# Kernel tuning notes

Measured on AMD Instinct MI355X. Metric: run time of the kernel, lower is better.

Reference implementation:

```python
import jax, jax.numpy as jnp
import numpy as np

MARGIN = 0.5
CURV = 1.0
B, D = 8192, 128
N_CLASSES = 256


def setup_inputs() -> dict:
    key = jax.random.key(0)
    k1, k2, k3 = jax.random.split(key, 3)
    emb = jax.random.normal(k1, (B, D), dtype=jnp.float32)
    # project onto Poincare ball: random radii in (0, 0.8) so all norms < 1
    radii = 0.8 * jax.random.uniform(k2, (B, 1), dtype=jnp.float32)
    emb = emb / (jnp.linalg.norm(emb, axis=-1, keepdims=True) + 1e-6) * radii
    labels = jax.random.randint(k3, (B,), 0, N_CLASSES, dtype=jnp.int64)
    return {"embeddings": emb, "labels": labels}


def _poincare_dist_matrix(x, c):
    # d(x,y) = arccosh(1 + 2c||x-y||^2 / ((1-c||x||^2)(1-c||y||^2))) / sqrt(c)
    sq = jnp.sum(x * x, axis=-1)                       # (B,)
    gram = x @ x.T                                      # (B,B) GEMM
    d2 = jnp.maximum(sq[:, None] + sq[None, :] - 2.0 * gram, 0.0)
    denom = (1.0 - c * sq)[:, None] * (1.0 - c * sq)[None, :]
    arg = 1.0 + 2.0 * c * d2 / denom
    # clamp slightly above 1: arccosh grad is infinite at 1 (diagonal / identical pts)
    return jnp.arccosh(jnp.maximum(arg, 1.0 + 1e-7)) / jnp.sqrt(c)


def reference(embeddings, labels):
    dist = _poincare_dist_matrix(embeddings, CURV)      # (B,B)
    same = labels[:, None] == labels[None, :]
    eye = jnp.eye(labels.shape[0], dtype=bool)
    pos_mask = same & ~eye
    neg_mask = ~same
    has_pos = jnp.any(pos_mask, axis=1)
    has_neg = jnp.any(neg_mask, axis=1)
    valid = has_pos & has_neg
    d_pos = jnp.max(jnp.where(pos_mask, dist, -jnp.inf), axis=1)
    d_neg = jnp.min(jnp.where(neg_mask, dist, jnp.inf), axis=1)
    d_pos = jnp.where(has_pos, d_pos, 0.0)
    d_neg = jnp.where(has_neg, d_neg, 0.0)
    l = jnp.maximum(d_pos - d_neg + MARGIN, 0.0)
    l = jnp.where(valid, l, 0.0)
    cnt = jnp.sum(valid)
    return jnp.where(cnt > 0, jnp.sum(l) / jnp.maximum(cnt, 1), 0.0)
```

## Files before the change

kernel.cpp:

```cpp
#include <hip/hip_runtime.h>
#include <hip/hip_bf16.h>

typedef __attribute__((ext_vector_type(8))) __bf16 bf16x8;
typedef __attribute__((ext_vector_type(4))) float f32x4;
typedef unsigned short u16;

#define NB 8192
#define ND 128
#define NCHUNK 8

__device__ inline u16 f2b(float f){
  __hip_bfloat16 h = __float2bfloat16(f);
  return *reinterpret_cast<u16*>(&h);
}

extern "C" __global__ __launch_bounds__(256)
void prep_k(const float* __restrict__ x, u16* __restrict__ xb,
            float* __restrict__ sq, float* __restrict__ pinv)
{
  const int tid = blockIdx.x * 256 + threadIdx.x;
  const int row = tid >> 5;
  const int sub = tid & 31;
  const float4 v = reinterpret_cast<const float4*>(x)[row * 32 + sub];
  float s = v.x*v.x + v.y*v.y + v.z*v.z + v.w*v.w;
  #pragma unroll
  for (int m = 1; m < 32; m <<= 1) s += __shfl_xor(s, m, 32);
  ushort4 o;
  o.x = f2b(v.x); o.y = f2b(v.y); o.z = f2b(v.z); o.w = f2b(v.w);
  reinterpret_cast<ushort4*>(xb)[row * 32 + sub] = o;
  if (sub == 0){ sq[row] = s; pinv[row] = 1.0f / (1.0f - s); }
}

extern "C" __global__ __launch_bounds__(256, 2)
void gram_k(const u16* __restrict__ xb, const float* __restrict__ sq,
            const float* __restrict__ pinv, const int* __restrict__ lab,
            float* __restrict__ ppos, float* __restrict__ pneg)
{
  __shared__ u16 Bt[128 * 128];
  const int wid  = threadIdx.x >> 6;
  const int lane = threadIdx.x & 63;
  const int m16  = lane & 15;
  const int quad = lane >> 4;
  const int R0 = blockIdx.x * 128;
  const int C0 = blockIdx.y * 1024;
  const int WR0 = R0 + wid * 32;

  bf16x8 afrag[2][4];
  #pragma unroll
  for (int mt = 0; mt < 2; ++mt){
    const u16* arow = xb + (WR0 + mt*16 + m16) * ND;
    #pragma unroll
    for (int ks = 0; ks < 4; ++ks)
      afrag[mt][ks] = *reinterpret_cast<const bf16x8*>(arow + ks*32 + quad*8);
  }

  float sqi[8]; int labi[8];
  #pragma unroll
  for (int mt = 0; mt < 2; ++mt)
    #pragma unroll
    for (int r = 0; r < 4; ++r){
      const int row = WR0 + mt*16 + quad*4 + r;
      sqi[mt*4+r]  = sq[row];
      labi[mt*4+r] = lab[row];
    }

  float vpos[8], vneg[8];
  #pragma unroll
  for (int i = 0; i < 8; ++i){ vpos[i] = -__builtin_inff(); vneg[i] = __builtin_inff(); }

  for (int ct = 0; ct < 8; ++ct){
    const int CT0 = C0 + ct * 128;
    __syncthreads();
    #pragma unroll
    for (int c = 0; c < 8; ++c){
      const int cc   = wid * 8 + c;
      const int brow = cc * 4 + (lane >> 4);
      const int src  = (lane & 15) ^ (brow & 15);
      const u16* gsrc = xb + (CT0 + brow) * ND + src * 8;
      __builtin_amdgcn_global_load_lds(
          (__attribute__((address_space(1))) void*)gsrc,
          (__attribute__((address_space(3))) void*)(Bt + cc * 512), 16, 0, 0);
    }
    __syncthreads();

    f32x4 acc[2][8];
    #pragma unroll
    for (int mt = 0; mt < 2; ++mt)
      #pragma unroll
      for (int nt = 0; nt < 8; ++nt){
        f32x4 z = {0.f, 0.f, 0.f, 0.f};
        acc[mt][nt] = z;
      }

    #pragma unroll
    for (int ks = 0; ks < 4; ++ks){
      const int t = ks * 4 + quad;
      #pragma unroll
      for (int nt = 0; nt < 8; ++nt){
        const bf16x8 bfrag = *reinterpret_cast<const bf16x8*>(
            Bt + (nt*16 + m16) * 128 + ((t ^ m16) * 8));
        acc[0][nt] = __builtin_amdgcn_mfma_f32_16x16x32_bf16(afrag[0][ks], bfrag, acc[0][nt], 0, 0, 0);
        acc[1][nt] = __builtin_amdgcn_mfma_f32_16x16x32_bf16(afrag[1][ks], bfrag, acc[1][nt], 0, 0, 0);
      }
    }

    #pragma unroll
    for (int nt = 0; nt < 8; ++nt){
      const int col  = CT0 + nt*16 + m16;
      const float sqj = sq[col];
      const float pj  = pinv[col];
      const int  labj = lab[col];
      #pragma unroll
      for (int mt = 0; mt < 2; ++mt){
        const bool tilediag = (WR0 + mt*16) == (CT0 + nt*16);
        #pragma unroll
        for (int r = 0; r < 4; ++r){
          const float g = acc[mt][nt][r];
          float u = fmaf(-2.0f, g, sqi[mt*4+r] + sqj);
          u = fmaxf(u, 0.0f) * pj;
          const bool same = (labi[mt*4+r] == labj);
          const bool dg   = tilediag && (m16 == quad*4 + r);
          const int idx = mt*4 + r;
          if (same && !dg) vpos[idx] = fmaxf(vpos[idx], u);
          if (!same)       vneg[idx] = fminf(vneg[idx], u);
        }
      }
    }
  }

  #pragma unroll
  for (int i = 0; i < 8; ++i){
    #pragma unroll
    for (int m = 1; m < 16; m <<= 1){
      vpos[i] = fmaxf(vpos[i], __shfl_xor(vpos[i], m, 16));
      vneg[i] = fminf(vneg[i], __shfl_xor(vneg[i], m, 16));
    }
  }
  if (m16 == 0){
    #pragma unroll
    for (int i = 0; i < 8; ++i){
      const int row = WR0 + (i >> 2)*16 + quad*4 + (i & 3);
      ppos[blockIdx.y * NB + row] = vpos[i];
      pneg[blockIdx.y * NB + row] = vneg[i];
    }
  }
}

extern "C" __global__ __launch_bounds__(1024)
void finalize_k(const float* __restrict__ ppos, const float* __restrict__ pneg,
                const float* __restrict__ pinv, float* __restrict__ out)
{
  float lsum = 0.0f; int lcnt = 0;
  for (int row = threadIdx.x; row < NB; row += 1024){
    float up = -__builtin_inff(), un = __builtin_inff();
    #pragma unroll
    for (int c = 0; c < NCHUNK; ++c){
      up = fmaxf(up, ppos[c * NB + row]);
      un = fminf(un, pneg[c * NB + row]);
    }
    const bool hp = (up > -__builtin_inff());
    const bool hn = (un <  __builtin_inff());
    const float pi = pinv[row];
    float dp = 0.0f, dn = 0.0f;
    if (hp){ float t = fmaxf(2.0f * up * pi, 1e-7f); dp = log1pf(t + sqrtf(t * (t + 2.0f))); }
    if (hn){ float t = fmaxf(2.0f * un * pi, 1e-7f); dn = log1pf(t + sqrtf(t * (t + 2.0f))); }
    if (hp && hn){ lsum += fmaxf(dp - dn + 0.5f, 0.0f); lcnt++; }
  }
  #pragma unroll
  for (int m = 1; m < 64; m <<= 1){
    lsum += __shfl_xor(lsum, m, 64);
    lcnt += __shfl_xor(lcnt, m, 64);
  }
  __shared__ float s_sum[16];
  __shared__ int   s_cnt[16];
  const int w = threadIdx.x >> 6;
  if ((threadIdx.x & 63) == 0){ s_sum[w] = lsum; s_cnt[w] = lcnt; }
  __syncthreads();
  if (threadIdx.x == 0){
    float S = 0.0f; int C = 0;
    for (int i = 0; i < 16; ++i){ S += s_sum[i]; C += s_cnt[i]; }
    out[0] = (C > 0) ? (S / (float)C) : 0.0f;
  }
}

extern "C" void kernel_launch(void* const* d_in, const int* in_sizes, int n_in,
                              void* d_out, int out_size, void* d_ws, size_t ws_size,
                              hipStream_t stream)
{
  const float* x  = (const float*)d_in[0];
  const int* lab  = (const int*)d_in[1];
  char* ws = (char*)d_ws;
  u16*  xb   = (u16*)ws;
  float* sq   = (float*)(ws + 2*1024*1024);
  float* pinv = (float*)(ws + 2*1024*1024 + 32*1024);
  float* ppos = (float*)(ws + 2*1024*1024 + 64*1024);
  float* pneg = (float*)(ws + 2*1024*1024 + 64*1024 + 256*1024);

  hipLaunchKernelGGL(prep_k, dim3(1024), dim3(256), 0, stream, x, xb, sq, pinv);
  hipLaunchKernelGGL(gram_k, dim3(64, NCHUNK), dim3(256), 0, stream,
                     xb, sq, pinv, lab, ppos, pneg);
  hipLaunchKernelGGL(finalize_k, dim3(1), dim3(1024), 0, stream, ppos, pneg, pinv, (float*)d_out);
}
```

Baseline: 116.7 us.

## Double gram grid chunks, pack column params, split epilogue, parallelize finalize

```diff
diff --git a/kernel.cpp b/kernel.cpp
--- a/kernel.cpp
+++ b/kernel.cpp
@@ -7,7 +7,9 @@
 
 #define NB 8192
 #define ND 128
-#define NCHUNK 8
+#define NCHUNK 16
+#define NEGINF (-__builtin_inff())
+#define POSINF (__builtin_inff())
 
 __device__ inline u16 f2b(float f){
   __hip_bfloat16 h = __float2bfloat16(f);
@@ -15,8 +17,8 @@
 }
 
 extern "C" __global__ __launch_bounds__(256)
-void prep_k(const float* __restrict__ x, u16* __restrict__ xb,
-            float* __restrict__ sq, float* __restrict__ pinv)
+void prep_k(const float* __restrict__ x, const int* __restrict__ lab,
+            u16* __restrict__ xb, float4* __restrict__ colp)
 {
   const int tid = blockIdx.x * 256 + threadIdx.x;
   const int row = tid >> 5;
@@ -28,12 +30,14 @@
   ushort4 o;
   o.x = f2b(v.x); o.y = f2b(v.y); o.z = f2b(v.z); o.w = f2b(v.w);
   reinterpret_cast<ushort4*>(xb)[row * 32 + sub] = o;
-  if (sub == 0){ sq[row] = s; pinv[row] = 1.0f / (1.0f - s); }
-}
-
-extern "C" __global__ __launch_bounds__(256, 2)
-void gram_k(const u16* __restrict__ xb, const float* __restrict__ sq,
-            const float* __restrict__ pinv, const int* __restrict__ lab,
+  if (sub == 0){
+    const float p = 1.0f / (1.0f - s);
+    colp[row] = make_float4(s, p, s * p, __int_as_float(lab[row]));
+  }
+}
+
+extern "C" __global__ __launch_bounds__(256, 4)
+void gram_k(const u16* __restrict__ xb, const float4* __restrict__ colp,
             float* __restrict__ ppos, float* __restrict__ pneg)
 {
   __shared__ u16 Bt[128 * 128];
@@ -41,8 +45,8 @@
   const int lane = threadIdx.x & 63;
   const int m16  = lane & 15;
   const int quad = lane >> 4;
-  const int R0 = blockIdx.x * 128;
-  const int C0 = blockIdx.y * 1024;
+  const int R0  = blockIdx.x * 128;
+  const int C0  = blockIdx.y * 512;
   const int WR0 = R0 + wid * 32;
 
   bf16x8 afrag[2][4];
@@ -59,23 +63,23 @@
   for (int mt = 0; mt < 2; ++mt)
     #pragma unroll
     for (int r = 0; r < 4; ++r){
-      const int row = WR0 + mt*16 + quad*4 + r;
-      sqi[mt*4+r]  = sq[row];
-      labi[mt*4+r] = lab[row];
+      const float4 cp = colp[WR0 + mt*16 + quad*4 + r];
+      sqi[mt*4+r]  = cp.x;
+      labi[mt*4+r] = __float_as_int(cp.w);
     }
 
   float vpos[8], vneg[8];
   #pragma unroll
-  for (int i = 0; i < 8; ++i){ vpos[i] = -__builtin_inff(); vneg[i] = __builtin_inff(); }
-
-  for (int ct = 0; ct < 8; ++ct){
+  for (int i = 0; i < 8; ++i){ vpos[i] = NEGINF; vneg[i] = POSINF; }
+
+  for (int ct = 0; ct < 4; ++ct){
     const int CT0 = C0 + ct * 128;
     __syncthreads();
     #pragma unroll
     for (int c = 0; c < 8; ++c){
       const int cc   = wid * 8 + c;
-      const int brow = cc * 4 + (lane >> 4);
-      const int src  = (lane & 15) ^ (brow & 15);
+      const int brow = cc * 4 + quad;
+      const int src  = m16 ^ (brow & 15);
       const u16* gsrc = xb + (CT0 + brow) * ND + src * 8;
       __builtin_amdgcn_global_load_lds(
           (__attribute__((address_space(1))) void*)gsrc,
@@ -83,46 +87,61 @@
     }
     __syncthreads();
 
-    f32x4 acc[2][8];
-    #pragma unroll
-    for (int mt = 0; mt < 2; ++mt)
+    #pragma unroll
+    for (int half = 0; half < 2; ++half){
+      f32x4 acc[2][4];
       #pragma unroll
-      for (int nt = 0; nt < 8; ++nt){
-        f32x4 z = {0.f, 0.f, 0.f, 0.f};
-        acc[mt][nt] = z;
+      for (int mt = 0; mt < 2; ++mt)
+        #pragma unroll
+        for (int nt4 = 0; nt4 < 4; ++nt4){
+          f32x4 z = {0.f, 0.f, 0.f, 0.f};
+          acc[mt][nt4] = z;
+        }
+
+      #pragma unroll
+      for (int ks = 0; ks < 4; ++ks){
+        const int t = ks * 4 + quad;
+        #pragma unroll
+        for (int nt4 = 0; nt4 < 4; ++nt4){
+          const int nt = half * 4 + nt4;
+          const bf16x8 bfrag = *reinterpret_cast<const bf16x8*>(
+              Bt + (nt*16 + m16) * 128 + ((t ^ m16) * 8));
+          acc[0][nt4] = __builtin_amdgcn_mfma_f32_16x16x32_bf16(afrag[0][ks], bfrag, acc[0][nt4], 0, 0, 0);
+          acc[1][nt4] = __builtin_amdgcn_mfma_f32_16x16x32_bf16(afrag[1][ks], bfrag, acc[1][nt4], 0, 0, 0);
+        }
       }
 
-    #pragma unroll
-    for (int ks = 0; ks < 4; ++ks){
-      const int t = ks * 4 + quad;
       #pragma unroll
-      for (int nt = 0; nt < 8; ++nt){
-        const bf16x8 bfrag = *reinterpret_cast<const bf16x8*>(
-            Bt + (nt*16 + m16) * 128 + ((t ^ m16) * 8));
-        acc[0][nt] = __builtin_amdgcn_mfma_f32_16x16x32_bf16(afrag[0][ks], bfrag, acc[0][nt], 0, 0, 0);
-        acc[1][nt] = __builtin_amdgcn_mfma_f32_16x16x32_bf16(afrag[1][ks], bfrag, acc[1][nt], 0, 0, 0);
-      }
-    }
-
-    #pragma unroll
-    for (int nt = 0; nt < 8; ++nt){
-      const int col  = CT0 + nt*16 + m16;
-      const float sqj = sq[col];
-      const float pj  = pinv[col];
-      const int  labj = lab[col];
-      #pragma unroll
-      for (int mt = 0; mt < 2; ++mt){
-        const bool tilediag = (WR0 + mt*16) == (CT0 + nt*16);
+      for (int nt4 = 0; nt4 < 4; ++nt4){
+        const int nt  = half * 4 + nt4;
+        const float4 cp = colp[CT0 + nt*16 + m16];
+        const float pj   = cp.y;
+        const float spj  = cp.z;
+        const int   labj = __float_as_int(cp.w);
+        const float n2pj = -2.0f * pj;
         #pragma unroll
-        for (int r = 0; r < 4; ++r){
-          const float g = acc[mt][nt][r];
-          float u = fmaf(-2.0f, g, sqi[mt*4+r] + sqj);
-          u = fmaxf(u, 0.0f) * pj;
-          const bool same = (labi[mt*4+r] == labj);
-          const bool dg   = tilediag && (m16 == quad*4 + r);
-          const int idx = mt*4 + r;
-          if (same && !dg) vpos[idx] = fmaxf(vpos[idx], u);
-          if (!same)       vneg[idx] = fminf(vneg[idx], u);
+        for (int mt = 0; mt < 2; ++mt){
+          const bool tilediag = (WR0 + mt*16) == (CT0 + nt*16);
+          if (!tilediag){
+            #pragma unroll
+            for (int r = 0; r < 4; ++r){
+              const int idx = mt*4 + r;
+              const float u = fmaf(n2pj, acc[mt][nt4][r], fmaf(sqi[idx], pj, spj));
+              const bool sm = (labi[idx] == labj);
+              vpos[idx] = fmaxf(vpos[idx], sm ? u : NEGINF);
+              vneg[idx] = fminf(vneg[idx], sm ? POSINF : u);
+            }
+          } else {
+            #pragma unroll
+            for (int r = 0; r < 4; ++r){
+              const int idx = mt*4 + r;
+              const float u = fmaf(n2pj, acc[mt][nt4][r], fmaf(sqi[idx], pj, spj));
+              const bool sm = (labi[idx] == labj);
+              const bool dg = (m16 == quad*4 + r);
+              vpos[idx] = fmaxf(vpos[idx], (sm && !dg) ? u : NEGINF);
+              vneg[idx] = fminf(vneg[idx], sm ? POSINF : u);
+            }
+          }
         }
       }
     }
@@ -146,41 +165,49 @@
   }
 }
 
-extern "C" __global__ __launch_bounds__(1024)
-void finalize_k(const float* __restrict__ ppos, const float* __restrict__ pneg,
-                const float* __restrict__ pinv, float* __restrict__ out)
-{
-  float lsum = 0.0f; int lcnt = 0;
-  for (int row = threadIdx.x; row < NB; row += 1024){
-    float up = -__builtin_inff(), un = __builtin_inff();
-    #pragma unroll
-    for (int c = 0; c < NCHUNK; ++c){
-      up = fmaxf(up, ppos[c * NB + row]);
-      un = fminf(un, pneg[c * NB + row]);
-    }
-    const bool hp = (up > -__builtin_inff());
-    const bool hn = (un <  __builtin_inff());
-    const float pi = pinv[row];
-    float dp = 0.0f, dn = 0.0f;
-    if (hp){ float t = fmaxf(2.0f * up * pi, 1e-7f); dp = log1pf(t + sqrtf(t * (t + 2.0f))); }
-    if (hn){ float t = fmaxf(2.0f * un * pi, 1e-7f); dn = log1pf(t + sqrtf(t * (t + 2.0f))); }
-    if (hp && hn){ lsum += fmaxf(dp - dn + 0.5f, 0.0f); lcnt++; }
-  }
+extern "C" __global__ __launch_bounds__(128)
+void fin1_k(const float* __restrict__ ppos, const float* __restrict__ pneg,
+            const float4* __restrict__ colp, float2* __restrict__ bpart)
+{
+  const int row = blockIdx.x * 128 + threadIdx.x;
+  float up = NEGINF, un = POSINF;
+  #pragma unroll
+  for (int c = 0; c < NCHUNK; ++c){
+    up = fmaxf(up, ppos[c * NB + row]);
+    un = fminf(un, pneg[c * NB + row]);
+  }
+  const bool hp = (up > NEGINF);
+  const bool hn = (un < POSINF);
+  const float pi = colp[row].y;
+  float dp = 0.0f, dn = 0.0f;
+  if (hp){ float t = fmaxf(2.0f * up * pi, 1e-7f); dp = log1pf(t + sqrtf(t * (t + 2.0f))); }
+  if (hn){ float t = fmaxf(2.0f * un * pi, 1e-7f); dn = log1pf(t + sqrtf(t * (t + 2.0f))); }
+  float lsum = (hp && hn) ? fmaxf(dp - dn + 0.5f, 0.0f) : 0.0f;
+  float lcnt = (hp && hn) ? 1.0f : 0.0f;
   #pragma unroll
   for (int m = 1; m < 64; m <<= 1){
     lsum += __shfl_xor(lsum, m, 64);
     lcnt += __shfl_xor(lcnt, m, 64);
   }
-  __shared__ float s_sum[16];
-  __shared__ int   s_cnt[16];
-  const int w = threadIdx.x >> 6;
-  if ((threadIdx.x & 63) == 0){ s_sum[w] = lsum; s_cnt[w] = lcnt; }
+  __shared__ float2 s_p[2];
+  if ((threadIdx.x & 63) == 0) s_p[threadIdx.x >> 6] = make_float2(lsum, lcnt);
   __syncthreads();
   if (threadIdx.x == 0){
-    float S = 0.0f; int C = 0;
-    for (int i = 0; i < 16; ++i){ S += s_sum[i]; C += s_cnt[i]; }
-    out[0] = (C > 0) ? (S / (float)C) : 0.0f;
-  }
+    bpart[blockIdx.x] = make_float2(s_p[0].x + s_p[1].x, s_p[0].y + s_p[1].y);
+  }
+}
+
+extern "C" __global__ __launch_bounds__(64)
+void fin2_k(const float2* __restrict__ bpart, float* __restrict__ out)
+{
+  float2 p = bpart[threadIdx.x];
+  float s = p.x, c = p.y;
+  #pragma unroll
+  for (int m = 1; m < 64; m <<= 1){
+    s += __shfl_xor(s, m, 64);
+    c += __shfl_xor(c, m, 64);
+  }
+  if (threadIdx.x == 0) out[0] = (c > 0.0f) ? (s / c) : 0.0f;
 }
 
 extern "C" void kernel_launch(void* const* d_in, const int* in_sizes, int n_in,
@@ -190,14 +217,15 @@
   const float* x  = (const float*)d_in[0];
   const int* lab  = (const int*)d_in[1];
   char* ws = (char*)d_ws;
-  u16*  xb   = (u16*)ws;
-  float* sq   = (float*)(ws + 2*1024*1024);
-  float* pinv = (float*)(ws + 2*1024*1024 + 32*1024);
-  float* ppos = (float*)(ws + 2*1024*1024 + 64*1024);
-  float* pneg = (float*)(ws + 2*1024*1024 + 64*1024 + 256*1024);
-
-  hipLaunchKernelGGL(prep_k, dim3(1024), dim3(256), 0, stream, x, xb, sq, pinv);
+  u16*    xb   = (u16*)ws;
+  float4* colp = (float4*)(ws + (size_t)2*1024*1024);
+  float*  ppos = (float*)(ws + (size_t)2*1024*1024 + 128*1024);
+  float*  pneg = (float*)(ws + (size_t)2*1024*1024 + 128*1024 + 512*1024);
+  float2* bpart= (float2*)(ws + (size_t)2*1024*1024 + 128*1024 + 1024*1024);
+
+  hipLaunchKernelGGL(prep_k, dim3(1024), dim3(256), 0, stream, x, lab, xb, colp);
   hipLaunchKernelGGL(gram_k, dim3(64, NCHUNK), dim3(256), 0, stream,
-                     xb, sq, pinv, lab, ppos, pneg);
-  hipLaunchKernelGGL(finalize_k, dim3(1), dim3(1024), 0, stream, ppos, pneg, pinv, (float*)d_out);
-}
+                     xb, colp, ppos, pneg);
+  hipLaunchKernelGGL(fin1_k, dim3(64), dim3(128), 0, stream, ppos, pneg, colp, bpart);
+  hipLaunchKernelGGL(fin2_k, dim3(1), dim3(64), 0, stream, bpart, (float*)d_out);
+}
```

New measurement: 102.3 us. 12.3% less time.
